# Kernel tuning notes

Measured on AMD Instinct MI355X. Metric: run time of the kernel, lower is better.

## Reference

```python
import jax, jax.numpy as jnp
import numpy as np

H = 12  # num_heads


def rotate_half(x):
    x1, x2 = jnp.split(x, 2, axis=-1)
    return jnp.concatenate([-x2, x1], axis=-1)


def setup_inputs() -> dict:
    key = jax.random.key(0)
    ks = jax.random.split(key, 8)
    B, N, C = 4, 2048, 768
    num_special = 5
    Ns = N - num_special
    D = C // H
    x = jax.random.normal(ks[0], (B, N, C), dtype=jnp.float32)
    rope_cos = jax.random.uniform(ks[1], (Ns, D), dtype=jnp.float32)
    rope_sin = jax.random.uniform(ks[2], (Ns, D), dtype=jnp.float32)
    W_qkv = jax.random.normal(ks[3], (C, 3 * C), dtype=jnp.float32) * (C ** -0.5)
    b_qkv = jax.random.normal(ks[4], (3 * C,), dtype=jnp.float32) * 0.02
    W_proj = jax.random.normal(ks[5], (C, C), dtype=jnp.float32) * (C ** -0.5)
    b_proj = jax.random.normal(ks[6], (C,), dtype=jnp.float32) * 0.02
    return {"x": x, "rope_cos": rope_cos, "rope_sin": rope_sin,
            "W_qkv": W_qkv, "b_qkv": b_qkv, "W_proj": W_proj, "b_proj": b_proj,
            "num_special": num_special}


def reference(x, rope_cos, rope_sin, W_qkv, b_qkv, W_proj, b_proj, num_special):
    B, N, C = x.shape
    D = C // H
    scale = D ** -0.5
    qkv = (x @ W_qkv + b_qkv).reshape(B, N, 3, H, D)
    qkv = jnp.transpose(qkv, (2, 0, 3, 1, 4))  # [3, B, H, N, D]
    q, k, v = qkv[0], qkv[1], qkv[2]
    # partial RoPE: special tokens untouched, spatial tokens rotated
    q_spec, q_spat = q[:, :, :num_special], q[:, :, num_special:]
    k_spec, k_spat = k[:, :, :num_special], k[:, :, num_special:]
    q_spat = q_spat * rope_cos + rotate_half(q_spat) * rope_sin
    k_spat = k_spat * rope_cos + rotate_half(k_spat) * rope_sin
    q = jnp.concatenate([q_spec, q_spat], axis=2)
    k = jnp.concatenate([k_spec, k_spat], axis=2)
    attn = jnp.einsum('bhqd,bhkd->bhqk', q, k) * scale  # [B,H,N,N]
    attn = jax.nn.softmax(attn, axis=-1)
    out = jnp.einsum('bhqk,bhkd->bhqd', attn, v)  # [B,H,N,D]
    out = jnp.transpose(out, (0, 2, 1, 3)).reshape(B, N, C)
    return out @ W_proj + b_proj
```

## Files before the change

kernel.cpp:

```cpp
#include <hip/hip_runtime.h>
#include <stdint.h>

typedef unsigned short u16;
typedef __bf16 bf16x8 __attribute__((ext_vector_type(8)));
typedef short s16x4 __attribute__((ext_vector_type(4)));
typedef float f32x4 __attribute__((ext_vector_type(4)));

typedef __attribute__((address_space(1))) void gvoid_t;
typedef __attribute__((address_space(3))) void lvoid_t;

struct alignas(16) U128 { uint32_t x, y, z, w; };
struct alignas(16) F128 { float x, y, z, w; };
struct alignas(8)  U64v { uint32_t x, y; };

__device__ __forceinline__ void gld16(const u16* g, u16* lds) {
  __builtin_amdgcn_global_load_lds((gvoid_t*)const_cast<u16*>(g),
                                   (lvoid_t*)lds, 16, 0, 0);
}

__device__ __forceinline__ u16 f2bf(float f) {
  uint32_t u = __builtin_bit_cast(uint32_t, f);
  u += 0x7FFFu + ((u >> 16) & 1u);
  return (u16)(u >> 16);
}
__device__ __forceinline__ float bf2f(u16 h) {
  return __builtin_bit_cast(float, (uint32_t)h << 16);
}
__device__ __forceinline__ bf16x8 ldfrag(const u16* p) {
  U128 u = *reinterpret_cast<const U128*>(p);
  return __builtin_bit_cast(bf16x8, u);
}
__device__ __forceinline__ uint32_t pkbf(float a, float b) {
  uint32_t ua = __builtin_bit_cast(uint32_t, a) + 0x8000u;
  uint32_t ub = __builtin_bit_cast(uint32_t, b) + 0x8000u;
  return (ua >> 16) | (ub & 0xFFFF0000u);
}

__device__ __forceinline__ float EXP2(float x) { return __builtin_amdgcn_exp2f(x); }

__global__ void cvt_f32_bf16(const float* __restrict__ in, u16* __restrict__ out) {
  int i = (blockIdx.x * 256 + threadIdx.x) * 4;
  F128 v = *reinterpret_cast<const F128*>(in + i);
  U64v o;
  o.x = (uint32_t)f2bf(v.x) | ((uint32_t)f2bf(v.y) << 16);
  o.y = (uint32_t)f2bf(v.z) | ((uint32_t)f2bf(v.w) << 16);
  *reinterpret_cast<U64v*>(out + i) = o;
}

__global__ void transpose_cvt(const float* __restrict__ W, u16* __restrict__ Wt,
                              int K, int N) {
  __shared__ float T[32][33];
  const int n0 = blockIdx.x * 32, k0 = blockIdx.y * 32;
  const int tid = threadIdx.x;
#pragma unroll
  for (int i = 0; i < 4; ++i) {
    int e = i * 256 + tid, r = e >> 5, c = e & 31;
    T[r][c] = W[(size_t)(k0 + r) * N + n0 + c];
  }
  __syncthreads();
#pragma unroll
  for (int i = 0; i < 4; ++i) {
    int e = i * 256 + tid, r = e >> 5, c = e & 31;
    Wt[(size_t)(n0 + r) * K + k0 + c] = f2bf(T[c][r]);
  }
}

template <int BF16_OUT>
__global__ __launch_bounds__(256, 2)
void gemm_bt(const u16* __restrict__ A, const u16* __restrict__ Bt,
             const float* __restrict__ bias, void* __restrict__ C,
             int M, int N, int K) {
  __shared__ u16 As[128 * 32];
  __shared__ u16 Bs[128 * 32];
  const int tid = threadIdx.x;
  const int wave = tid >> 6, lane = tid & 63;
  const int quad = lane >> 4, l16 = lane & 15;
  const int m0 = blockIdx.y * 128, n0 = blockIdx.x * 128;
  const int wr = (wave & 1) * 64, wc = (wave >> 1) * 64;

  f32x4 acc[4][4];
#pragma unroll
  for (int i = 0; i < 4; ++i)
#pragma unroll
    for (int j = 0; j < 4; ++j) acc[i][j] = (f32x4){0.f, 0.f, 0.f, 0.f};

  for (int k0 = 0; k0 < K; k0 += 32) {
    __syncthreads();
#pragma unroll
    for (int j = 0; j < 2; ++j) {
      int c = (wave * 2 + j) * 64 + lane;
      int row = c >> 2, kq = c & 3;
      gld16(A + (size_t)(m0 + row) * K + k0 + kq * 8, &As[(wave * 2 + j) * 512]);
      gld16(Bt + (size_t)(n0 + row) * K + k0 + kq * 8, &Bs[(wave * 2 + j) * 512]);
    }
    __syncthreads();
    bf16x8 af[4], bfr[4];
#pragma unroll
    for (int rb = 0; rb < 4; ++rb) af[rb] = ldfrag(&As[(wr + rb * 16 + l16) * 32 + quad * 8]);
#pragma unroll
    for (int cb = 0; cb < 4; ++cb) bfr[cb] = ldfrag(&Bs[(wc + cb * 16 + l16) * 32 + quad * 8]);
#pragma unroll
    for (int rb = 0; rb < 4; ++rb)
#pragma unroll
      for (int cb = 0; cb < 4; ++cb)
        acc[rb][cb] = __builtin_amdgcn_mfma_f32_16x16x32_bf16(af[rb], bfr[cb], acc[rb][cb], 0, 0, 0);
  }
#pragma unroll
  for (int cb = 0; cb < 4; ++cb) {
    int col = n0 + wc + cb * 16 + l16;
    float bv = bias[col];
#pragma unroll
    for (int rb = 0; rb < 4; ++rb) {
#pragma unroll
      for (int r = 0; r < 4; ++r) {
        int row = m0 + wr + rb * 16 + quad * 4 + r;
        float v = acc[rb][cb][r] + bv;
        if constexpr (BF16_OUT)
          ((u16*)C)[(size_t)row * N + col] = f2bf(v);
        else
          ((float*)C)[(size_t)row * N + col] = v;
      }
    }
  }
}

__global__ void rope_scatter(const u16* __restrict__ qkvb,
                             const float* __restrict__ cosT, const float* __restrict__ sinT,
                             const int* __restrict__ nsp,
                             u16* __restrict__ Qo, u16* __restrict__ Ko, u16* __restrict__ Vto) {
  __shared__ float Vls[64][65];
  const int tid = threadIdx.x;
  const int t0 = blockIdx.x * 64, h = blockIdx.y, b = blockIdx.z;
  const int bh = b * 12 + h;
  const int num_special = nsp[0];
  const float QS = 0.125f * 1.4426950408889634f;

#pragma unroll
  for (int s = 0; s < 2; ++s) {
    const int base_col = s * 768 + h * 64;
    u16* outp = s ? Ko : Qo;
    const float qs = s ? 1.0f : QS;
#pragma unroll
    for (int i = 0; i < 8; ++i) {
      int pid = i * 256 + tid;
      int t = pid >> 5, dp = pid & 31;
      int n = t0 + t;
      size_t m = (size_t)b * 2048 + n;
      float x1 = bf2f(qkvb[m * 2304 + base_col + dp]);
      float x2 = bf2f(qkvb[m * 2304 + base_col + dp + 32]);
      float o1, o2;
      if (n < num_special) {
        o1 = x1; o2 = x2;
      } else {
        int ns = n - num_special;
        float c1 = cosT[ns * 64 + dp],      s1 = sinT[ns * 64 + dp];
        float c2 = cosT[ns * 64 + dp + 32], s2 = sinT[ns * 64 + dp + 32];
        o1 = x1 * c1 - x2 * s1;
        o2 = x2 * c2 + x1 * s2;
      }
      size_t ob = ((size_t)bh * 2048 + n) * 64;
      outp[ob + dp] = f2bf(o1 * qs);
      outp[ob + dp + 32] = f2bf(o2 * qs);
    }
  }
#pragma unroll
  for (int i = 0; i < 16; ++i) {
    int e = i * 256 + tid, t = e >> 6, d = e & 63;
    size_t m = (size_t)b * 2048 + t0 + t;
    Vls[t][d] = bf2f(qkvb[m * 2304 + 1536 + h * 64 + d]);
  }
  __syncthreads();
#pragma unroll
  for (int i = 0; i < 16; ++i) {
    int e = i * 256 + tid, d = e >> 6, t = e & 63;
    Vto[((size_t)bh * 64 + d) * 2048 + t0 + t] = f2bf(Vls[t][d]);
  }
}

__global__ __launch_bounds__(256, 3)
void attn(const u16* __restrict__ Q, const u16* __restrict__ Kg,
          const u16* __restrict__ Vt, u16* __restrict__ Out) {
  __shared__ u16 smem[2 * 64 * 72];
  __shared__ float invS[64];
  u16* Ks = smem;
  u16* Vs = smem + 64 * 72;
  u16* Qs = smem;
  const int tid = threadIdx.x;
  const int wave = tid >> 6, lane = tid & 63;
  const int quad = lane >> 4, l16 = lane & 15;
  const int idx = blockIdx.x;
  const int bh = idx % 48, qt = idx / 48;
  const int b = bh / 12, h = bh % 12;
  const u16* Qb = Q + (size_t)bh * 2048 * 64;
  const u16* Kb = Kg + (size_t)bh * 2048 * 64;
  const u16* Vb = Vt + (size_t)bh * 64 * 2048;
  const int wkey0 = wave * 16;

#pragma unroll
  for (int j = 0; j < 2; ++j) {
    int c = j * 256 + tid;
    int row = c >> 3, kq = c & 7;
    *(U128*)&Qs[row * 72 + kq * 8] =
        *(const U128*)(Qb + (size_t)(qt * 64 + row) * 64 + kq * 8);
  }
  __syncthreads();
  bf16x8 qf[4][2];
#pragma unroll
  for (int m = 0; m < 4; ++m) {
    qf[m][0] = ldfrag(&Qs[(m * 16 + l16) * 72 + quad * 8]);
    qf[m][1] = ldfrag(&Qs[(m * 16 + l16) * 72 + quad * 8 + 32]);
  }

  f32x4 oacc[4][4];
#pragma unroll
  for (int m = 0; m < 4; ++m)
#pragma unroll
    for (int db = 0; db < 4; ++db) oacc[m][db] = (f32x4){0.f, 0.f, 0.f, 0.f};
  float psum[4] = {0.f, 0.f, 0.f, 0.f};

  for (int kt = 0; kt < 32; ++kt) {
    __syncthreads();
#pragma unroll
    for (int j = 0; j < 2; ++j) {
      int c = j * 256 + tid;
      int row = c >> 3, kq = c & 7;
      *(U128*)&Ks[row * 72 + kq * 8] =
          *(const U128*)(Kb + (size_t)(kt * 64 + row) * 64 + kq * 8);
      *(U128*)&Vs[row * 72 + kq * 8] =
          *(const U128*)(Vb + (size_t)row * 2048 + kt * 64 + kq * 8);
    }
    __syncthreads();

    bf16x8 ka0 = ldfrag(&Ks[(wkey0 + l16) * 72 + quad * 8]);
    bf16x8 ka1 = ldfrag(&Ks[(wkey0 + l16) * 72 + quad * 8 + 32]);

    s16x4 pf[4];
#pragma unroll
    for (int m = 0; m < 4; ++m) {
      f32x4 st = (f32x4){0.f, 0.f, 0.f, 0.f};
      st = __builtin_amdgcn_mfma_f32_16x16x32_bf16(ka0, qf[m][0], st, 0, 0, 0);
      st = __builtin_amdgcn_mfma_f32_16x16x32_bf16(ka1, qf[m][1], st, 0, 0, 0);
      float p0 = EXP2(st[0]);
      float p1 = EXP2(st[1]);
      float p2 = EXP2(st[2]);
      float p3 = EXP2(st[3]);
      psum[m] += (p0 + p1) + (p2 + p3);
      U64v pd;
      pd.x = pkbf(p0, p1);
      pd.y = pkbf(p2, p3);
      pf[m] = __builtin_bit_cast(s16x4, pd);
    }

#pragma unroll
    for (int db = 0; db < 4; ++db) {
      s16x4 vf = __builtin_bit_cast(s16x4,
          *(const U64v*)&Vs[(db * 16 + l16) * 72 + wkey0 + quad * 4]);
#pragma unroll
      for (int m = 0; m < 4; ++m)
        oacc[m][db] = __builtin_amdgcn_mfma_f32_16x16x16bf16_1k(pf[m], vf, oacc[m][db], 0, 0, 0);
    }
  }

#pragma unroll
  for (int m = 0; m < 4; ++m) {
    psum[m] += __shfl_xor(psum[m], 16, 64);
    psum[m] += __shfl_xor(psum[m], 32, 64);
  }
  __syncthreads();
  float* LS = (float*)smem;
  if (quad == 0) {
#pragma unroll
    for (int m = 0; m < 4; ++m) LS[wave * 64 + m * 16 + l16] = psum[m];
  }
  __syncthreads();
  if (tid < 64) {
    float tot = LS[tid] + LS[64 + tid] + LS[128 + tid] + LS[192 + tid];
    invS[tid] = 1.0f / tot;
  }

  float* OR = (float*)smem;
  const int q = tid >> 2;
  const int d0 = (tid & 3) * 4;
  const size_t obase = ((size_t)(b * 2048 + qt * 64 + q)) * 768 + h * 64 + d0;
#pragma unroll
  for (int db = 0; db < 4; ++db) {
    __syncthreads();
#pragma unroll
    for (int m = 0; m < 4; ++m)
#pragma unroll
      for (int r = 0; r < 4; ++r)
        OR[(wave * 64 + m * 16 + quad * 4 + r) * 18 + l16] = oacc[m][db][r];
    __syncthreads();
    float s0 = 0.f, s1 = 0.f, s2 = 0.f, s3 = 0.f;
#pragma unroll
    for (int w = 0; w < 4; ++w) {
      const float* p = &OR[(w * 64 + q) * 18 + d0];
      s0 += p[0]; s1 += p[1]; s2 += p[2]; s3 += p[3];
    }
    float iv = invS[q];
    U64v o;
    o.x = (uint32_t)f2bf(s0 * iv) | ((uint32_t)f2bf(s1 * iv) << 16);
    o.y = (uint32_t)f2bf(s2 * iv) | ((uint32_t)f2bf(s3 * iv) << 16);
    *(U64v*)&Out[obase + db * 16] = o;
  }
}

extern "C" void kernel_launch(void* const* d_in, const int* in_sizes, int n_in,
                              void* d_out, int out_size, void* d_ws, size_t ws_size,
                              hipStream_t stream) {
  (void)in_sizes; (void)n_in; (void)out_size; (void)ws_size;
  const float* x        = (const float*)d_in[0];
  const float* rope_cos = (const float*)d_in[1];
  const float* rope_sin = (const float*)d_in[2];
  const float* W_qkv    = (const float*)d_in[3];
  const float* b_qkv    = (const float*)d_in[4];
  const float* W_proj   = (const float*)d_in[5];
  const float* b_proj   = (const float*)d_in[6];
  const int*   nsp      = (const int*)d_in[7];
  float* out = (float*)d_out;

  char* ws = (char*)d_ws;
  u16* Xb   = (u16*)(ws);
  u16* Wqkt = (u16*)(ws + 12582912);
  u16* Wpt  = (u16*)(ws + 16121856);
  u16* qkvb = (u16*)(ws + 17301504);
  u16* Qb   = (u16*)(ws + 55050240);
  u16* Kb   = (u16*)(ws + 67633152);
  u16* Vtb  = (u16*)(ws + 80216064);
  u16* att  = (u16*)(ws + 92798976);

  cvt_f32_bf16<<<6144, 256, 0, stream>>>(x, Xb);
  transpose_cvt<<<dim3(72, 24), 256, 0, stream>>>(W_qkv, Wqkt, 768, 2304);
  transpose_cvt<<<dim3(24, 24), 256, 0, stream>>>(W_proj, Wpt, 768, 768);
  gemm_bt<1><<<dim3(18, 64), 256, 0, stream>>>(Xb, Wqkt, b_qkv, qkvb, 8192, 2304, 768);
  rope_scatter<<<dim3(32, 12, 4), 256, 0, stream>>>(qkvb, rope_cos, rope_sin, nsp, Qb, Kb, Vtb);
  attn<<<1536, 256, 0, stream>>>(Qb, Kb, Vtb, att);
  gemm_bt<0><<<dim3(6, 64), 256, 0, stream>>>(att, Wpt, b_proj, out, 8192, 768, 768);
}
```

Baseline: 259.5 us.

## Fuse QKV projection GEMM with RoPE, head scatter and V transpose epilogue

The QKV GEMM epilogue now applies bias, partial RoPE and Q scaling, and writes Q/K straight into per-head layout and V in transposed layout. This drops the separate rope_scatter kernel and the bf16 qkv intermediate round trip through global memory. In exchange the epilogue writes are less coalesced: 2-byte scattered stores for Q/K and 8-byte strided stores for V.

```diff
diff --git a/kernel.cpp b/kernel.cpp
--- a/kernel.cpp
+++ b/kernel.cpp
@@ -65,10 +65,9 @@
   }
 }
 
-template <int BF16_OUT>
 __global__ __launch_bounds__(256, 2)
 void gemm_bt(const u16* __restrict__ A, const u16* __restrict__ Bt,
-             const float* __restrict__ bias, void* __restrict__ C,
+             const float* __restrict__ bias, float* __restrict__ C,
              int M, int N, int K) {
   __shared__ u16 As[128 * 32];
   __shared__ u16 Bs[128 * 32];
@@ -114,66 +113,112 @@
 #pragma unroll
       for (int r = 0; r < 4; ++r) {
         int row = m0 + wr + rb * 16 + quad * 4 + r;
-        float v = acc[rb][cb][r] + bv;
-        if constexpr (BF16_OUT)
-          ((u16*)C)[(size_t)row * N + col] = f2bf(v);
-        else
-          ((float*)C)[(size_t)row * N + col] = v;
+        C[(size_t)row * N + col] = acc[rb][cb][r] + bv;
       }
     }
   }
 }
 
-__global__ void rope_scatter(const u16* __restrict__ qkvb,
-                             const float* __restrict__ cosT, const float* __restrict__ sinT,
-                             const int* __restrict__ nsp,
-                             u16* __restrict__ Qo, u16* __restrict__ Ko, u16* __restrict__ Vto) {
-  __shared__ float Vls[64][65];
+__global__ __launch_bounds__(256, 2)
+void gemm_qkv_rope(const u16* __restrict__ A, const u16* __restrict__ Bt,
+                   const float* __restrict__ bias,
+                   const float* __restrict__ cosT, const float* __restrict__ sinT,
+                   const int* __restrict__ nsp,
+                   u16* __restrict__ Qo, u16* __restrict__ Ko, u16* __restrict__ Vto) {
+  __shared__ u16 As[128 * 32];
+  __shared__ u16 Bs[128 * 32];
+  const int K = 768, N = 2304;
   const int tid = threadIdx.x;
-  const int t0 = blockIdx.x * 64, h = blockIdx.y, b = blockIdx.z;
-  const int bh = b * 12 + h;
+  const int wave = tid >> 6, lane = tid & 63;
+  const int quad = lane >> 4, l16 = lane & 15;
+  const int m0 = blockIdx.y * 128, n0 = blockIdx.x * 128;
+  const int wr = (wave & 1) * 64, wc = (wave >> 1) * 64;
+
+  f32x4 acc[4][4];
+#pragma unroll
+  for (int i = 0; i < 4; ++i)
+#pragma unroll
+    for (int j = 0; j < 4; ++j) acc[i][j] = (f32x4){0.f, 0.f, 0.f, 0.f};
+
+  for (int k0 = 0; k0 < K; k0 += 32) {
+    __syncthreads();
+#pragma unroll
+    for (int j = 0; j < 2; ++j) {
+      int c = (wave * 2 + j) * 64 + lane;
+      int row = c >> 2, kq = c & 3;
+      gld16(A + (size_t)(m0 + row) * K + k0 + kq * 8, &As[(wave * 2 + j) * 512]);
+      gld16(Bt + (size_t)(n0 + row) * K + k0 + kq * 8, &Bs[(wave * 2 + j) * 512]);
+    }
+    __syncthreads();
+    bf16x8 af[4], bfr[4];
+#pragma unroll
+    for (int rb = 0; rb < 4; ++rb) af[rb] = ldfrag(&As[(wr + rb * 16 + l16) * 32 + quad * 8]);
+#pragma unroll
+    for (int cb = 0; cb < 4; ++cb) bfr[cb] = ldfrag(&Bs[(wc + cb * 16 + l16) * 32 + quad * 8]);
+#pragma unroll
+    for (int rb = 0; rb < 4; ++rb)
+#pragma unroll
+      for (int cb = 0; cb < 4; ++cb)
+        acc[rb][cb] = __builtin_amdgcn_mfma_f32_16x16x32_bf16(af[rb], bfr[cb], acc[rb][cb], 0, 0, 0);
+  }
+
+  const int sec = blockIdx.x / 6;
+  const int gcol0 = n0 + wc;
+  const int hh = (gcol0 >> 6) % 12;
+  const int bb = m0 >> 11;
+  const int nbase = m0 & 2047;
+  const int bh = bb * 12 + hh;
   const int num_special = nsp[0];
   const float QS = 0.125f * 1.4426950408889634f;
 
-#pragma unroll
-  for (int s = 0; s < 2; ++s) {
-    const int base_col = s * 768 + h * 64;
-    u16* outp = s ? Ko : Qo;
-    const float qs = s ? 1.0f : QS;
-#pragma unroll
-    for (int i = 0; i < 8; ++i) {
-      int pid = i * 256 + tid;
-      int t = pid >> 5, dp = pid & 31;
-      int n = t0 + t;
-      size_t m = (size_t)b * 2048 + n;
-      float x1 = bf2f(qkvb[m * 2304 + base_col + dp]);
-      float x2 = bf2f(qkvb[m * 2304 + base_col + dp + 32]);
-      float o1, o2;
-      if (n < num_special) {
-        o1 = x1; o2 = x2;
-      } else {
-        int ns = n - num_special;
-        float c1 = cosT[ns * 64 + dp],      s1 = sinT[ns * 64 + dp];
-        float c2 = cosT[ns * 64 + dp + 32], s2 = sinT[ns * 64 + dp + 32];
-        o1 = x1 * c1 - x2 * s1;
-        o2 = x2 * c2 + x1 * s2;
+  if (sec < 2) {
+    u16* outp = sec ? Ko : Qo;
+    const float qs = sec ? 1.0f : QS;
+#pragma unroll
+    for (int cbp = 0; cbp < 2; ++cbp) {
+      const int d1 = cbp * 16 + l16;
+      const int d2 = d1 + 32;
+      const float bv1 = bias[gcol0 + d1];
+      const float bv2 = bias[gcol0 + d2];
+#pragma unroll
+      for (int rb = 0; rb < 4; ++rb) {
+#pragma unroll
+        for (int r = 0; r < 4; ++r) {
+          const int n = nbase + wr + rb * 16 + quad * 4 + r;
+          float v1 = acc[rb][cbp][r] + bv1;
+          float v2 = acc[rb][cbp + 2][r] + bv2;
+          float o1, o2;
+          if (n < num_special) {
+            o1 = v1; o2 = v2;
+          } else {
+            int ns = n - num_special;
+            float c1 = cosT[ns * 64 + d1], s1 = sinT[ns * 64 + d1];
+            float c2 = cosT[ns * 64 + d2], s2 = sinT[ns * 64 + d2];
+            o1 = v1 * c1 - v2 * s1;
+            o2 = v2 * c2 + v1 * s2;
+          }
+          size_t ob = ((size_t)bh * 2048 + n) * 64;
+          outp[ob + d1] = f2bf(o1 * qs);
+          outp[ob + d2] = f2bf(o2 * qs);
+        }
       }
-      size_t ob = ((size_t)bh * 2048 + n) * 64;
-      outp[ob + dp] = f2bf(o1 * qs);
-      outp[ob + dp + 32] = f2bf(o2 * qs);
-    }
-  }
-#pragma unroll
-  for (int i = 0; i < 16; ++i) {
-    int e = i * 256 + tid, t = e >> 6, d = e & 63;
-    size_t m = (size_t)b * 2048 + t0 + t;
-    Vls[t][d] = bf2f(qkvb[m * 2304 + 1536 + h * 64 + d]);
-  }
-  __syncthreads();
-#pragma unroll
-  for (int i = 0; i < 16; ++i) {
-    int e = i * 256 + tid, d = e >> 6, t = e & 63;
-    Vto[((size_t)bh * 64 + d) * 2048 + t0 + t] = f2bf(Vls[t][d]);
+    }
+  } else {
+#pragma unroll
+    for (int cb = 0; cb < 4; ++cb) {
+      const int d = cb * 16 + l16;
+      const float bv = bias[gcol0 + d];
+#pragma unroll
+      for (int rb = 0; rb < 4; ++rb) {
+        const int nr = nbase + wr + rb * 16 + quad * 4;
+        U64v o;
+        o.x = (uint32_t)f2bf(acc[rb][cb][0] + bv) |
+              ((uint32_t)f2bf(acc[rb][cb][1] + bv) << 16);
+        o.y = (uint32_t)f2bf(acc[rb][cb][2] + bv) |
+              ((uint32_t)f2bf(acc[rb][cb][3] + bv) << 16);
+        *(U64v*)&Vto[((size_t)bh * 64 + d) * 2048 + nr] = o;
+      }
+    }
   }
 }
 
@@ -323,7 +368,6 @@
   u16* Xb   = (u16*)(ws);
   u16* Wqkt = (u16*)(ws + 12582912);
   u16* Wpt  = (u16*)(ws + 16121856);
-  u16* qkvb = (u16*)(ws + 17301504);
   u16* Qb   = (u16*)(ws + 55050240);
   u16* Kb   = (u16*)(ws + 67633152);
   u16* Vtb  = (u16*)(ws + 80216064);
@@ -332,8 +376,8 @@
   cvt_f32_bf16<<<6144, 256, 0, stream>>>(x, Xb);
   transpose_cvt<<<dim3(72, 24), 256, 0, stream>>>(W_qkv, Wqkt, 768, 2304);
   transpose_cvt<<<dim3(24, 24), 256, 0, stream>>>(W_proj, Wpt, 768, 768);
-  gemm_bt<1><<<dim3(18, 64), 256, 0, stream>>>(Xb, Wqkt, b_qkv, qkvb, 8192, 2304, 768);
-  rope_scatter<<<dim3(32, 12, 4), 256, 0, stream>>>(qkvb, rope_cos, rope_sin, nsp, Qb, Kb, Vtb);
+  gemm_qkv_rope<<<dim3(18, 64), 256, 0, stream>>>(Xb, Wqkt, b_qkv, rope_cos, rope_sin,
+                                                  nsp, Qb, Kb, Vtb);
   attn<<<1536, 256, 0, stream>>>(Qb, Kb, Vtb, att);
-  gemm_bt<0><<<dim3(6, 64), 256, 0, stream>>>(att, Wpt, b_proj, out, 8192, 768, 768);
-}
+  gemm_bt<<<dim3(6, 64), 256, 0, stream>>>(att, Wpt, b_proj, out, 8192, 768, 768);
+}
```

New measurement: 249.3 us. 4.0% less time.
